# Kernel tuning notes

Hardware: AMD Instinct MI355X
Metric: run time of the kernel (lower is better)

## Reference

```python
import jax, jax.numpy as jnp
import numpy as np

N_NODES = 100000
N_EDGES = 1600000
IN_DIM, HID, OUT_DIM = 128, 64, 1


def _sage_conv(x, src, dst, wl, wr, b, num_nodes):
    # PyG SAGEConv (aggr='mean', root_weight=True):
    #   out = lin_l(mean_{j in N(i)} x_j) + lin_r(x_i), bias lives in lin_l
    msgs = x[src]                                                  # [E, d] gather
    agg = jax.ops.segment_sum(msgs, dst, num_segments=num_nodes)  # [N, d]
    deg = jax.ops.segment_sum(jnp.ones((src.shape[0],), x.dtype), dst,
                              num_segments=num_nodes)              # [N]
    agg = agg / jnp.maximum(deg, 1.0)[:, None]                     # mean aggregation
    return agg @ wl + x @ wr + b


def setup_inputs() -> dict:
    key = jax.random.key(0)
    ks = jax.random.split(key, 12)
    x = jax.random.normal(ks[0], (N_NODES, IN_DIM), dtype=jnp.float32)
    edge_index = jax.random.randint(ks[1], (2, N_EDGES), 0, N_NODES, dtype=jnp.int64)

    def glorot(k, fan_in, fan_out):
        s = jnp.sqrt(2.0 / (fan_in + fan_out)).astype(jnp.float32)
        return jax.random.normal(k, (fan_in, fan_out), dtype=jnp.float32) * s

    return {
        "x": x,
        "edge_index": edge_index,
        "wl0": glorot(ks[2], IN_DIM, HID), "wr0": glorot(ks[3], IN_DIM, HID),
        "b0": jnp.zeros((HID,), jnp.float32),
        "wl1": glorot(ks[4], HID, HID), "wr1": glorot(ks[5], HID, HID),
        "b1": jnp.zeros((HID,), jnp.float32),
        "wl2": glorot(ks[6], HID, OUT_DIM), "wr2": glorot(ks[7], HID, OUT_DIM),
        "b2": jnp.zeros((OUT_DIM,), jnp.float32),
    }


def reference(x, edge_index, wl0, wr0, b0, wl1, wr1, b1, wl2, wr2, b2):
    src, dst = edge_index[0], edge_index[1]
    n = x.shape[0]
    # layer 0: conv -> relu (dropout is identity in eval mode)
    h = jax.nn.relu(_sage_conv(x, src, dst, wl0, wr0, b0, n))
    # layer 1
    h = jax.nn.relu(_sage_conv(h, src, dst, wl1, wr1, b1, n))
    # final layer + sigmoid
    h = _sage_conv(h, src, dst, wl2, wr2, b2, n)
    return jax.nn.sigmoid(h)
```

## Files before the change

kernel.cpp:

```cpp
#include <hip/hip_runtime.h>
#include <hip/hip_bf16.h>
#include <math.h>


#define SHIFT 7
#define BKT 128
#define CHUNK 4096

typedef __bf16 bf16_t;
typedef bf16_t bf16x8 __attribute__((ext_vector_type(8)));
typedef float f32x4 __attribute__((ext_vector_type(4)));

#define B16LO(u) __uint_as_float((u) << 16)
#define B16HI(u) __uint_as_float((u) & 0xffff0000u)

__global__ __launch_bounds__(256) void hist_bucket(const int* __restrict__ dstv,
                                                   int* __restrict__ bucket_cnt,
                                                   int E, int NB, int nbC,
                                                   const float* __restrict__ wl0,
                                                   const float* __restrict__ wr0,
                                                   const float* __restrict__ wl1,
                                                   const float* __restrict__ wr1,
                                                   bf16_t* __restrict__ w0t,
                                                   bf16_t* __restrict__ w1t) {
    if ((int)blockIdx.x >= nbC) {
        int idx = (blockIdx.x - nbC) * 256 + threadIdx.x;
        if (idx < 128 * 128) {
            int j = idx >> 7, k = idx & 127;
            float v = (j < 64) ? wl0[k * 64 + j] : wr0[k * 64 + (j - 64)];
            w0t[idx] = (bf16_t)v;
        } else if (idx < 128 * 128 + 128 * 64) {
            int i2 = idx - 128 * 128;
            int j = i2 >> 6, k = i2 & 63;
            float v = (j < 64) ? wl1[k * 64 + j] : wr1[k * 64 + (j - 64)];
            w1t[i2] = (bf16_t)v;
        }
        return;
    }
    __shared__ int h[1024];
    for (int i = threadIdx.x; i < NB; i += 256) h[i] = 0;
    __syncthreads();
    int base = blockIdx.x * CHUNK;
#pragma unroll
    for (int k = 0; k < CHUNK / 256; ++k) {
        int e = base + threadIdx.x + k * 256;
        if (e < E) atomicAdd(&h[dstv[e] >> SHIFT], 1);
    }
    __syncthreads();
    for (int i = threadIdx.x; i < NB; i += 256)
        if (h[i]) atomicAdd(&bucket_cnt[i], h[i]);
}

__global__ __launch_bounds__(1024) void scan_bucket(const int* __restrict__ cnt,
                                                    int* __restrict__ boff,
                                                    int* __restrict__ bcur, int NB) {
    __shared__ int s[1024];
    int t = threadIdx.x;
    int v = (t < NB) ? cnt[t] : 0;
    s[t] = v;
    __syncthreads();
    for (int d = 1; d < 1024; d <<= 1) {
        int x = (t >= d) ? s[t - d] : 0;
        __syncthreads();
        s[t] += x;
        __syncthreads();
    }
    if (t < NB) {
        int o = s[t] - v;
        boff[t] = o;
        bcur[t] = o;
    }
    if (t == NB - 1) boff[NB] = s[t];
}

__global__ __launch_bounds__(256) void scatter_bucket(const int* __restrict__ srcv,
                                                      const int* __restrict__ dstv,
                                                      int* __restrict__ bcur,
                                                      int* __restrict__ bucketed,
                                                      int E, int NB) {
    __shared__ int hist[1024];
    __shared__ int offl[1024];
    __shared__ int basel[1024];
    __shared__ int partial[256];
    __shared__ int posA[CHUNK];
    __shared__ int valA[CHUNK];
    const int t = threadIdx.x;
    for (int i = t; i < NB; i += 256) hist[i] = 0;
    __syncthreads();

    const int cbase = blockIdx.x * CHUNK;
    int bk[CHUNK / 256], rk[CHUNK / 256], vv[CHUNK / 256];
#pragma unroll
    for (int k = 0; k < CHUNK / 256; ++k) {
        int e = cbase + t + k * 256;
        if (e < E) {
            int d = dstv[e];
            int s = srcv[e];
            int b = d >> SHIFT;
            bk[k] = b;
            rk[k] = atomicAdd(&hist[b], 1);
            vv[k] = (s << SHIFT) | (d & (BKT - 1));
        } else {
            bk[k] = -1;
        }
    }
    __syncthreads();

    for (int b = t; b < NB; b += 256) {
        int c = hist[b];
        basel[b] = c ? atomicAdd(&bcur[b], c) : 0;
    }
    {
        int g = t * 4;
        int a0 = (g + 0 < NB) ? hist[g + 0] : 0;
        int a1 = (g + 1 < NB) ? hist[g + 1] : 0;
        int a2 = (g + 2 < NB) ? hist[g + 2] : 0;
        int a3 = (g + 3 < NB) ? hist[g + 3] : 0;
        int sum = a0 + a1 + a2 + a3;
        partial[t] = sum;
        __syncthreads();
        for (int d = 1; d < 256; d <<= 1) {
            int x = (t >= d) ? partial[t - d] : 0;
            __syncthreads();
            partial[t] += x;
            __syncthreads();
        }
        int ex = partial[t] - sum;
        if (g + 0 < NB) offl[g + 0] = ex;
        if (g + 1 < NB) offl[g + 1] = ex + a0;
        if (g + 2 < NB) offl[g + 2] = ex + a0 + a1;
        if (g + 3 < NB) offl[g + 3] = ex + a0 + a1 + a2;
    }
    __syncthreads();

    int nloc = E - cbase;
    if (nloc > CHUNK) nloc = CHUNK;
#pragma unroll
    for (int k = 0; k < CHUNK / 256; ++k) {
        if (bk[k] >= 0) {
            int slot = offl[bk[k]] + rk[k];
            posA[slot] = basel[bk[k]] + rk[k];
            valA[slot] = vv[k];
        }
    }
    __syncthreads();
    for (int j = t; j < nloc; j += 256) bucketed[posA[j]] = valA[j];
}

__global__ __launch_bounds__(256) void sort_bucket(const int* __restrict__ bucketed,
                                                   const int* __restrict__ boff,
                                                   int2* __restrict__ od,
                                                   int* __restrict__ csr, int N) {
    __shared__ int cnt[BKT];
    __shared__ int sc[BKT];
    __shared__ int cur[BKT];
    const int b = blockIdx.x;
    const int t = threadIdx.x;
    const int ebase = boff[b], eend = boff[b + 1];
    if (t < BKT) cnt[t] = 0;
    __syncthreads();
    for (int i = ebase + t; i < eend; i += 256)
        atomicAdd(&cnt[bucketed[i] & (BKT - 1)], 1);
    __syncthreads();
    int v = (t < BKT) ? cnt[t] : 0;
    if (t < BKT) sc[t] = v;
    __syncthreads();
    for (int d = 1; d < BKT; d <<= 1) {
        int x = (t < BKT && t >= d) ? sc[t - d] : 0;
        __syncthreads();
        if (t < BKT) sc[t] += x;
        __syncthreads();
    }
    if (t < BKT) {
        int ex = sc[t] - v;
        cur[t] = ex;
        int dst = (b << SHIFT) + t;
        if (dst < N) od[dst] = make_int2(ebase + ex, v);
    }
    __syncthreads();
    for (int i = ebase + t; i < eend; i += 256) {
        int w = bucketed[i];
        int p = atomicAdd(&cur[w & (BKT - 1)], 1);
        csr[ebase + p] = w >> SHIFT;
    }
}

template <int KTOT, bool AIN_BF16>
__global__ __launch_bounds__(256) void gemm_mfma(const void* __restrict__ Ain,
                                                 const bf16_t* __restrict__ Wt,
                                                 bf16_t* __restrict__ Y, int N) {
    const int lane = threadIdx.x & 63;
    const int wv = threadIdx.x >> 6;
    const int r0 = blockIdx.x * 64 + wv * 16;
    const int rr = lane & 15;
    const int quad = lane >> 4;
    const int row_store = r0 + rr;
    int row = (row_store < N) ? row_store : (N - 1);
    constexpr int NK = KTOT / 32;

    bf16x8 xf[NK];
    if (AIN_BF16) {
        const bf16_t* A = (const bf16_t*)Ain;
#pragma unroll
        for (int kk = 0; kk < NK; ++kk)
            xf[kk] = *(const bf16x8*)&A[(size_t)row * KTOT + kk * 32 + quad * 8];
    } else {
        const float* A = (const float*)Ain;
#pragma unroll
        for (int kk = 0; kk < NK; ++kk) {
            const float* ap = &A[(size_t)row * KTOT + kk * 32 + quad * 8];
            float4 f0 = *(const float4*)ap;
            float4 f1 = *(const float4*)(ap + 4);
            union { bf16x8 v; bf16_t h[8]; } u;
            u.h[0] = (bf16_t)f0.x; u.h[1] = (bf16_t)f0.y;
            u.h[2] = (bf16_t)f0.z; u.h[3] = (bf16_t)f0.w;
            u.h[4] = (bf16_t)f1.x; u.h[5] = (bf16_t)f1.y;
            u.h[6] = (bf16_t)f1.z; u.h[7] = (bf16_t)f1.w;
            xf[kk] = u.v;
        }
    }

#pragma unroll
    for (int c = 0; c < 8; ++c) {
        f32x4 acc = {0.f, 0.f, 0.f, 0.f};
#pragma unroll
        for (int kk = 0; kk < NK; ++kk) {
            bf16x8 wf = *(const bf16x8*)&Wt[(size_t)(c * 16 + rr) * KTOT + kk * 32 + quad * 8];
            acc = __builtin_amdgcn_mfma_f32_16x16x32_bf16(wf, xf[kk], acc, 0, 0, 0);
        }
        if (row_store < N) {
            union { bf16_t h[4]; uint2 u; } p;
            p.h[0] = (bf16_t)acc[0]; p.h[1] = (bf16_t)acc[1];
            p.h[2] = (bf16_t)acc[2]; p.h[3] = (bf16_t)acc[3];
            *(uint2*)&Y[(size_t)row_store * 128 + c * 16 + quad * 4] = p.u;
        }
    }
}

template <bool FUSED>
__global__ __launch_bounds__(256) void agg_relu(const bf16_t* __restrict__ y,
                                                const int* __restrict__ csr,
                                                const int2* __restrict__ od,
                                                const float* __restrict__ bias,
                                                bf16_t* __restrict__ h,
                                                const float* __restrict__ wl2,
                                                const float* __restrict__ wr2,
                                                float* __restrict__ sl,
                                                float* __restrict__ sr, int N) {
    const int lane = threadIdx.x & 63;
    const int oct = lane >> 3;
    const int ch = (lane & 7) * 8;
    const int nw = gridDim.x * 4;

    int i = blockIdx.x * 4 + (threadIdx.x >> 6);
    int2 odc = (i < N) ? od[i] : make_int2(0, 0);
    int sidx = 0;
    if (i < N) sidx = (lane < odc.y) ? csr[odc.x + lane] : 0;

    while (i < N) {
        const int inext = i + nw;
        int2 odn = (inext < N) ? od[inext] : make_int2(0, 0);

        const int base = odc.x;
        const int d = odc.y;
        float a0 = 0.f, a1 = 0.f, a2 = 0.f, a3 = 0.f;
        float a4 = 0.f, a5 = 0.f, a6 = 0.f, a7 = 0.f;
        const int nblk = d >> 3;
        const int pm = (nblk < 8) ? nblk : 8;
        int p = 0;
        for (; p + 2 <= pm; p += 2) {
            int s0 = __shfl(sidx, 8 * p + oct);
            int s1 = __shfl(sidx, 8 * p + 8 + oct);
            uint4 v0 = *(const uint4*)&y[(size_t)s0 * 128 + ch];
            uint4 v1 = *(const uint4*)&y[(size_t)s1 * 128 + ch];
            a0 += B16LO(v0.x) + B16LO(v1.x); a1 += B16HI(v0.x) + B16HI(v1.x);
            a2 += B16LO(v0.y) + B16LO(v1.y); a3 += B16HI(v0.y) + B16HI(v1.y);
            a4 += B16LO(v0.z) + B16LO(v1.z); a5 += B16HI(v0.z) + B16HI(v1.z);
            a6 += B16LO(v0.w) + B16LO(v1.w); a7 += B16HI(v0.w) + B16HI(v1.w);
        }
        for (; p < pm; ++p) {
            int s0 = __shfl(sidx, 8 * p + oct);
            uint4 v0 = *(const uint4*)&y[(size_t)s0 * 128 + ch];
            a0 += B16LO(v0.x); a1 += B16HI(v0.x);
            a2 += B16LO(v0.y); a3 += B16HI(v0.y);
            a4 += B16LO(v0.z); a5 += B16HI(v0.z);
            a6 += B16LO(v0.w); a7 += B16HI(v0.w);
        }
        for (; p < nblk; ++p) {
            int s0 = csr[base + 8 * p + oct];
            uint4 v0 = *(const uint4*)&y[(size_t)s0 * 128 + ch];
            a0 += B16LO(v0.x); a1 += B16HI(v0.x);
            a2 += B16LO(v0.y); a3 += B16HI(v0.y);
            a4 += B16LO(v0.z); a5 += B16HI(v0.z);
            a6 += B16LO(v0.w); a7 += B16HI(v0.w);
        }
        {
            int te = 8 * nblk + oct;
            int tec = (te < 64) ? te : 63;
            int s_t = __shfl(sidx, tec);
            if (te < d) {
                int s0 = (te < 64) ? s_t : csr[base + te];
                uint4 v0 = *(const uint4*)&y[(size_t)s0 * 128 + ch];
                a0 += B16LO(v0.x); a1 += B16HI(v0.x);
                a2 += B16LO(v0.y); a3 += B16HI(v0.y);
                a4 += B16LO(v0.z); a5 += B16HI(v0.z);
                a6 += B16LO(v0.w); a7 += B16HI(v0.w);
            }
        }

        int sidxn = 0;
        if (inext < N) sidxn = (lane < odn.y) ? csr[odn.x + lane] : 0;

        a0 += __shfl_xor(a0, 8);  a1 += __shfl_xor(a1, 8);
        a2 += __shfl_xor(a2, 8);  a3 += __shfl_xor(a3, 8);
        a4 += __shfl_xor(a4, 8);  a5 += __shfl_xor(a5, 8);
        a6 += __shfl_xor(a6, 8);  a7 += __shfl_xor(a7, 8);
        a0 += __shfl_xor(a0, 16); a1 += __shfl_xor(a1, 16);
        a2 += __shfl_xor(a2, 16); a3 += __shfl_xor(a3, 16);
        a4 += __shfl_xor(a4, 16); a5 += __shfl_xor(a5, 16);
        a6 += __shfl_xor(a6, 16); a7 += __shfl_xor(a7, 16);
        a0 += __shfl_xor(a0, 32); a1 += __shfl_xor(a1, 32);
        a2 += __shfl_xor(a2, 32); a3 += __shfl_xor(a3, 32);
        a4 += __shfl_xor(a4, 32); a5 += __shfl_xor(a5, 32);
        a6 += __shfl_xor(a6, 32); a7 += __shfl_xor(a7, 32);

        float inv = 1.f / ((d > 0) ? (float)d : 1.f);
        uint4 vs = *(const uint4*)&y[(size_t)i * 128 + 64 + ch];
        float4 bv0 = *(const float4*)&bias[ch];
        float4 bv1 = *(const float4*)&bias[ch + 4];
        float v0 = fmaxf(a0 * inv + B16LO(vs.x) + bv0.x, 0.f);
        float v1 = fmaxf(a1 * inv + B16HI(vs.x) + bv0.y, 0.f);
        float v2 = fmaxf(a2 * inv + B16LO(vs.y) + bv0.z, 0.f);
        float v3 = fmaxf(a3 * inv + B16HI(vs.y) + bv0.w, 0.f);
        float v4 = fmaxf(a4 * inv + B16LO(vs.z) + bv1.x, 0.f);
        float v5 = fmaxf(a5 * inv + B16HI(vs.z) + bv1.y, 0.f);
        float v6 = fmaxf(a6 * inv + B16LO(vs.w) + bv1.z, 0.f);
        float v7 = fmaxf(a7 * inv + B16HI(vs.w) + bv1.w, 0.f);

        if (!FUSED) {
            if (oct == 0) {
                union { bf16_t b[8]; uint4 u; } pk;
                pk.b[0] = (bf16_t)v0; pk.b[1] = (bf16_t)v1;
                pk.b[2] = (bf16_t)v2; pk.b[3] = (bf16_t)v3;
                pk.b[4] = (bf16_t)v4; pk.b[5] = (bf16_t)v5;
                pk.b[6] = (bf16_t)v6; pk.b[7] = (bf16_t)v7;
                *(uint4*)&h[(size_t)i * 64 + ch] = pk.u;
            }
        } else {
            float4 w0 = *(const float4*)&wl2[ch];
            float4 w1 = *(const float4*)&wl2[ch + 4];
            float4 u0 = *(const float4*)&wr2[ch];
            float4 u1 = *(const float4*)&wr2[ch + 4];
            float a = v0 * w0.x + v1 * w0.y + v2 * w0.z + v3 * w0.w +
                      v4 * w1.x + v5 * w1.y + v6 * w1.z + v7 * w1.w;
            float b = v0 * u0.x + v1 * u0.y + v2 * u0.z + v3 * u0.w +
                      v4 * u1.x + v5 * u1.y + v6 * u1.z + v7 * u1.w;
            a += __shfl_xor(a, 1); b += __shfl_xor(b, 1);
            a += __shfl_xor(a, 2); b += __shfl_xor(b, 2);
            a += __shfl_xor(a, 4); b += __shfl_xor(b, 4);
            if (lane == 0) { sl[i] = a; sr[i] = b; }
        }

        odc = odn;
        sidx = sidxn;
        i = inext;
    }
}

__global__ __launch_bounds__(256) void final_k(const float* __restrict__ sl,
                                               const float* __restrict__ sr,
                                               const int* __restrict__ csr,
                                               const int2* __restrict__ od,
                                               const float* __restrict__ b2,
                                               float* __restrict__ out, int N) {
    int wid = blockIdx.x * 4 + (threadIdx.x >> 6);
    if (wid >= N) return;
    const int lane = threadIdx.x & 63;
    const int2 odv = od[wid];
    const int base = odv.x;
    const int d = odv.y;
    float acc = 0.f;
    for (int e = lane; e < d; e += 64) acc += sl[csr[base + e]];
#pragma unroll
    for (int off = 32; off; off >>= 1) acc += __shfl_xor(acc, off);
    if (lane == 0) {
        float m = (d > 0) ? (float)d : 1.f;
        float v = acc / m + sr[wid] + b2[0];
        out[wid] = 1.f / (1.f + expf(-v));
    }
}

extern "C" void kernel_launch(void* const* d_in, const int* in_sizes, int n_in,
                              void* d_out, int out_size, void* d_ws, size_t ws_size,
                              hipStream_t stream) {
    const float* x  = (const float*)d_in[0];
    const int*  ei  = (const int*)d_in[1];
    const float* wl0 = (const float*)d_in[2];
    const float* wr0 = (const float*)d_in[3];
    const float* b0  = (const float*)d_in[4];
    const float* wl1 = (const float*)d_in[5];
    const float* wr1 = (const float*)d_in[6];
    const float* b1  = (const float*)d_in[7];
    const float* wl2 = (const float*)d_in[8];
    const float* wr2 = (const float*)d_in[9];
    const float* b2  = (const float*)d_in[10];
    float* out = (float*)d_out;

    const int E = in_sizes[1] / 2;
    const int N = out_size;
    const int* srcv = ei;
    const int* dstv = ei + E;
    const int NB = (N + BKT - 1) >> SHIFT;

    char* ws = (char*)d_ws;
    size_t o = 0;
    auto take = [&](size_t nbytes) -> void* {
        void* p = ws + o;
        o = (o + nbytes + 255) & ~(size_t)255;
        return p;
    };
    int2* od    = (int2*)take((size_t)N * 8);
    int* bcnt   = (int*)take((size_t)(NB + 2) * 4);
    int* boff   = (int*)take((size_t)(NB + 2) * 4);
    int* bcur   = (int*)take((size_t)(NB + 2) * 4);
    int* csr    = (int*)take((size_t)E * 4);
    bf16_t* w0t = (bf16_t*)take(128 * 128 * 2);
    bf16_t* w1t = (bf16_t*)take(128 * 64 * 2);
    bf16_t* y   = (bf16_t*)take((size_t)N * 128 * 2);
    bf16_t* h   = (bf16_t*)take((size_t)N * 64 * 2);
    float* sl   = (float*)take((size_t)N * 4);
    float* sr   = (float*)take((size_t)N * 4);
    int* bucketed = (int*)y;
    (void)ws_size;

    const int nbC = (E + CHUNK - 1) / CHUNK;
    const int nbP = (128 * 128 + 128 * 64 + 255) / 256;
    const int nbW = (N + 3) / 4;
    const int nbG = (N + 63) / 64;
    const int nbA = 2048;

    hipMemsetAsync(bcnt, 0, (size_t)NB * 4, stream);
    hist_bucket<<<nbC + nbP, 256, 0, stream>>>(dstv, bcnt, E, NB, nbC,
                                               wl0, wr0, wl1, wr1, w0t, w1t);
    scan_bucket<<<1, 1024, 0, stream>>>(bcnt, boff, bcur, NB);
    scatter_bucket<<<nbC, 256, 0, stream>>>(srcv, dstv, bcur, bucketed, E, NB);
    sort_bucket<<<NB, 256, 0, stream>>>(bucketed, boff, od, csr, N);

    gemm_mfma<128, false><<<nbG, 256, 0, stream>>>((const void*)x, w0t, y, N);
    agg_relu<false><<<nbA, 256, 0, stream>>>(y, csr, od, b0, h,
                                             nullptr, nullptr, nullptr, nullptr, N);
    gemm_mfma<64, true><<<nbG, 256, 0, stream>>>((const void*)h, w1t, y, N);
    agg_relu<true><<<nbA, 256, 0, stream>>>(y, csr, od, b1, nullptr,
                                            wl2, wr2, sl, sr, N);
    final_k<<<nbW, 256, 0, stream>>>(sl, sr, csr, od, b2, out, N);
}
```

Before: 313.8 us.

## Split GEMM output into separate left/right arrays, add nontemporal loads, halve chunk

The GEMM output is split into two contiguous N×64 arrays, one for the neighbour (lin_l) half and one for the root (lin_r) half. The gather in agg_relu then reads a compact 128-byte row per neighbour instead of half of a 256-byte interleaved row, which should improve cache-line use and L2 footprint. Streaming index, offset and CSR accesses now use nontemporal loads and stores to reduce cache pollution. The bucketing CHUNK is halved, giving more blocks and less shared memory per block. Nontemporal hints on reused data such as csr and od could hurt reuse across kernels.

```diff
diff --git a/kernel.cpp b/kernel.cpp
--- a/kernel.cpp
+++ b/kernel.cpp
@@ -5,7 +5,7 @@
 
 #define SHIFT 7
 #define BKT 128
-#define CHUNK 4096
+#define CHUNK 2048
 
 typedef __bf16 bf16_t;
 typedef bf16_t bf16x8 __attribute__((ext_vector_type(8)));
@@ -13,6 +13,23 @@
 
 #define B16LO(u) __uint_as_float((u) << 16)
 #define B16HI(u) __uint_as_float((u) & 0xffff0000u)
+
+__device__ __forceinline__ int ntload_i(const int* p) {
+    return __builtin_nontemporal_load(p);
+}
+__device__ __forceinline__ int2 ntload_i2(const int2* p) {
+    long long v = __builtin_nontemporal_load((const long long*)p);
+    return make_int2((int)(v & 0xffffffffll), (int)(v >> 32));
+}
+__device__ __forceinline__ uint4 ntload_u4(const void* p) {
+    const unsigned long long* q = (const unsigned long long*)p;
+    unsigned long long a = __builtin_nontemporal_load(q);
+    unsigned long long b = __builtin_nontemporal_load(q + 1);
+    uint4 r;
+    r.x = (uint)a; r.y = (uint)(a >> 32);
+    r.z = (uint)b; r.w = (uint)(b >> 32);
+    return r;
+}
 
 __global__ __launch_bounds__(256) void hist_bucket(const int* __restrict__ dstv,
                                                    int* __restrict__ bucket_cnt,
@@ -44,7 +61,7 @@
 #pragma unroll
     for (int k = 0; k < CHUNK / 256; ++k) {
         int e = base + threadIdx.x + k * 256;
-        if (e < E) atomicAdd(&h[dstv[e] >> SHIFT], 1);
+        if (e < E) atomicAdd(&h[ntload_i(&dstv[e]) >> SHIFT], 1);
     }
     __syncthreads();
     for (int i = threadIdx.x; i < NB; i += 256)
@@ -94,8 +111,8 @@
     for (int k = 0; k < CHUNK / 256; ++k) {
         int e = cbase + t + k * 256;
         if (e < E) {
-            int d = dstv[e];
-            int s = srcv[e];
+            int d = ntload_i(&dstv[e]);
+            int s = ntload_i(&srcv[e]);
             int b = d >> SHIFT;
             bk[k] = b;
             rk[k] = atomicAdd(&hist[b], 1);
@@ -144,7 +161,8 @@
         }
     }
     __syncthreads();
-    for (int j = t; j < nloc; j += 256) bucketed[posA[j]] = valA[j];
+    for (int j = t; j < nloc; j += 256)
+        __builtin_nontemporal_store(valA[j], &bucketed[posA[j]]);
 }
 
 __global__ __launch_bounds__(256) void sort_bucket(const int* __restrict__ bucketed,
@@ -160,7 +178,7 @@
     if (t < BKT) cnt[t] = 0;
     __syncthreads();
     for (int i = ebase + t; i < eend; i += 256)
-        atomicAdd(&cnt[bucketed[i] & (BKT - 1)], 1);
+        atomicAdd(&cnt[ntload_i(&bucketed[i]) & (BKT - 1)], 1);
     __syncthreads();
     int v = (t < BKT) ? cnt[t] : 0;
     if (t < BKT) sc[t] = v;
@@ -179,16 +197,17 @@
     }
     __syncthreads();
     for (int i = ebase + t; i < eend; i += 256) {
-        int w = bucketed[i];
+        int w = ntload_i(&bucketed[i]);
         int p = atomicAdd(&cur[w & (BKT - 1)], 1);
-        csr[ebase + p] = w >> SHIFT;
+        __builtin_nontemporal_store(w >> SHIFT, &csr[ebase + p]);
     }
 }
 
 template <int KTOT, bool AIN_BF16>
 __global__ __launch_bounds__(256) void gemm_mfma(const void* __restrict__ Ain,
                                                  const bf16_t* __restrict__ Wt,
-                                                 bf16_t* __restrict__ Y, int N) {
+                                                 bf16_t* __restrict__ Yl,
+                                                 bf16_t* __restrict__ Yr, int N) {
     const int lane = threadIdx.x & 63;
     const int wv = threadIdx.x >> 6;
     const int r0 = blockIdx.x * 64 + wv * 16;
@@ -232,13 +251,17 @@
             union { bf16_t h[4]; uint2 u; } p;
             p.h[0] = (bf16_t)acc[0]; p.h[1] = (bf16_t)acc[1];
             p.h[2] = (bf16_t)acc[2]; p.h[3] = (bf16_t)acc[3];
-            *(uint2*)&Y[(size_t)row_store * 128 + c * 16 + quad * 4] = p.u;
+            int col = c * 16 + quad * 4;
+            bf16_t* dp = (c < 4) ? &Yl[(size_t)row_store * 64 + col]
+                                 : &Yr[(size_t)row_store * 64 + (col - 64)];
+            *(uint2*)dp = p.u;
         }
     }
 }
 
 template <bool FUSED>
-__global__ __launch_bounds__(256) void agg_relu(const bf16_t* __restrict__ y,
+__global__ __launch_bounds__(256) void agg_relu(const bf16_t* __restrict__ yl,
+                                                const bf16_t* __restrict__ yr,
                                                 const int* __restrict__ csr,
                                                 const int2* __restrict__ od,
                                                 const float* __restrict__ bias,
@@ -253,13 +276,13 @@
     const int nw = gridDim.x * 4;
 
     int i = blockIdx.x * 4 + (threadIdx.x >> 6);
-    int2 odc = (i < N) ? od[i] : make_int2(0, 0);
+    int2 odc = (i < N) ? ntload_i2(&od[i]) : make_int2(0, 0);
     int sidx = 0;
-    if (i < N) sidx = (lane < odc.y) ? csr[odc.x + lane] : 0;
+    if (i < N) sidx = (lane < odc.y) ? ntload_i(&csr[odc.x + lane]) : 0;
 
     while (i < N) {
         const int inext = i + nw;
-        int2 odn = (inext < N) ? od[inext] : make_int2(0, 0);
+        int2 odn = (inext < N) ? ntload_i2(&od[inext]) : make_int2(0, 0);
 
         const int base = odc.x;
         const int d = odc.y;
@@ -271,8 +294,8 @@
         for (; p + 2 <= pm; p += 2) {
             int s0 = __shfl(sidx, 8 * p + oct);
             int s1 = __shfl(sidx, 8 * p + 8 + oct);
-            uint4 v0 = *(const uint4*)&y[(size_t)s0 * 128 + ch];
-            uint4 v1 = *(const uint4*)&y[(size_t)s1 * 128 + ch];
+            uint4 v0 = *(const uint4*)&yl[(size_t)s0 * 64 + ch];
+            uint4 v1 = *(const uint4*)&yl[(size_t)s1 * 64 + ch];
             a0 += B16LO(v0.x) + B16LO(v1.x); a1 += B16HI(v0.x) + B16HI(v1.x);
             a2 += B16LO(v0.y) + B16LO(v1.y); a3 += B16HI(v0.y) + B16HI(v1.y);
             a4 += B16LO(v0.z) + B16LO(v1.z); a5 += B16HI(v0.z) + B16HI(v1.z);
@@ -280,15 +303,15 @@
         }
         for (; p < pm; ++p) {
             int s0 = __shfl(sidx, 8 * p + oct);
-            uint4 v0 = *(const uint4*)&y[(size_t)s0 * 128 + ch];
+            uint4 v0 = *(const uint4*)&yl[(size_t)s0 * 64 + ch];
             a0 += B16LO(v0.x); a1 += B16HI(v0.x);
             a2 += B16LO(v0.y); a3 += B16HI(v0.y);
             a4 += B16LO(v0.z); a5 += B16HI(v0.z);
             a6 += B16LO(v0.w); a7 += B16HI(v0.w);
         }
         for (; p < nblk; ++p) {
-            int s0 = csr[base + 8 * p + oct];
-            uint4 v0 = *(const uint4*)&y[(size_t)s0 * 128 + ch];
+            int s0 = ntload_i(&csr[base + 8 * p + oct]);
+            uint4 v0 = *(const uint4*)&yl[(size_t)s0 * 64 + ch];
             a0 += B16LO(v0.x); a1 += B16HI(v0.x);
             a2 += B16LO(v0.y); a3 += B16HI(v0.y);
             a4 += B16LO(v0.z); a5 += B16HI(v0.z);
@@ -299,8 +322,8 @@
             int tec = (te < 64) ? te : 63;
             int s_t = __shfl(sidx, tec);
             if (te < d) {
-                int s0 = (te < 64) ? s_t : csr[base + te];
-                uint4 v0 = *(const uint4*)&y[(size_t)s0 * 128 + ch];
+                int s0 = (te < 64) ? s_t : ntload_i(&csr[base + te]);
+                uint4 v0 = *(const uint4*)&yl[(size_t)s0 * 64 + ch];
                 a0 += B16LO(v0.x); a1 += B16HI(v0.x);
                 a2 += B16LO(v0.y); a3 += B16HI(v0.y);
                 a4 += B16LO(v0.z); a5 += B16HI(v0.z);
@@ -309,7 +332,7 @@
         }
 
         int sidxn = 0;
-        if (inext < N) sidxn = (lane < odn.y) ? csr[odn.x + lane] : 0;
+        if (inext < N) sidxn = (lane < odn.y) ? ntload_i(&csr[odn.x + lane]) : 0;
 
         a0 += __shfl_xor(a0, 8);  a1 += __shfl_xor(a1, 8);
         a2 += __shfl_xor(a2, 8);  a3 += __shfl_xor(a3, 8);
@@ -325,7 +348,7 @@
         a6 += __shfl_xor(a6, 32); a7 += __shfl_xor(a7, 32);
 
         float inv = 1.f / ((d > 0) ? (float)d : 1.f);
-        uint4 vs = *(const uint4*)&y[(size_t)i * 128 + 64 + ch];
+        uint4 vs = ntload_u4(&yr[(size_t)i * 64 + ch]);
         float4 bv0 = *(const float4*)&bias[ch];
         float4 bv1 = *(const float4*)&bias[ch + 4];
         float v0 = fmaxf(a0 * inv + B16LO(vs.x) + bv0.x, 0.f);
@@ -344,7 +367,9 @@
                 pk.b[2] = (bf16_t)v2; pk.b[3] = (bf16_t)v3;
                 pk.b[4] = (bf16_t)v4; pk.b[5] = (bf16_t)v5;
                 pk.b[6] = (bf16_t)v6; pk.b[7] = (bf16_t)v7;
-                *(uint4*)&h[(size_t)i * 64 + ch] = pk.u;
+                unsigned long long* hp = (unsigned long long*)&h[(size_t)i * 64 + ch];
+                __builtin_nontemporal_store(((unsigned long long)pk.u.y << 32) | pk.u.x, hp);
+                __builtin_nontemporal_store(((unsigned long long)pk.u.w << 32) | pk.u.z, hp + 1);
             }
         } else {
             float4 w0 = *(const float4*)&wl2[ch];
@@ -376,11 +401,11 @@
     int wid = blockIdx.x * 4 + (threadIdx.x >> 6);
     if (wid >= N) return;
     const int lane = threadIdx.x & 63;
-    const int2 odv = od[wid];
+    const int2 odv = ntload_i2(&od[wid]);
     const int base = odv.x;
     const int d = odv.y;
     float acc = 0.f;
-    for (int e = lane; e < d; e += 64) acc += sl[csr[base + e]];
+    for (int e = lane; e < d; e += 64) acc += sl[ntload_i(&csr[base + e])];
 #pragma unroll
     for (int off = 32; off; off >>= 1) acc += __shfl_xor(acc, off);
     if (lane == 0) {
@@ -426,11 +451,12 @@
     int* csr    = (int*)take((size_t)E * 4);
     bf16_t* w0t = (bf16_t*)take(128 * 128 * 2);
     bf16_t* w1t = (bf16_t*)take(128 * 64 * 2);
-    bf16_t* y   = (bf16_t*)take((size_t)N * 128 * 2);
+    bf16_t* yl  = (bf16_t*)take((size_t)N * 64 * 2);
+    bf16_t* yr  = (bf16_t*)take((size_t)N * 64 * 2);
     bf16_t* h   = (bf16_t*)take((size_t)N * 64 * 2);
     float* sl   = (float*)take((size_t)N * 4);
     float* sr   = (float*)take((size_t)N * 4);
-    int* bucketed = (int*)y;
+    int* bucketed = (int*)yl;
     (void)ws_size;
 
     const int nbC = (E + CHUNK - 1) / CHUNK;
@@ -446,11 +472,11 @@
     scatter_bucket<<<nbC, 256, 0, stream>>>(srcv, dstv, bcur, bucketed, E, NB);
     sort_bucket<<<NB, 256, 0, stream>>>(bucketed, boff, od, csr, N);
 
-    gemm_mfma<128, false><<<nbG, 256, 0, stream>>>((const void*)x, w0t, y, N);
-    agg_relu<false><<<nbA, 256, 0, stream>>>(y, csr, od, b0, h,
+    gemm_mfma<128, false><<<nbG, 256, 0, stream>>>((const void*)x, w0t, yl, yr, N);
+    agg_relu<false><<<nbA, 256, 0, stream>>>(yl, yr, csr, od, b0, h,
                                              nullptr, nullptr, nullptr, nullptr, N);
-    gemm_mfma<64, true><<<nbG, 256, 0, stream>>>((const void*)h, w1t, y, N);
-    agg_relu<true><<<nbA, 256, 0, stream>>>(y, csr, od, b1, nullptr,
+    gemm_mfma<64, true><<<nbG, 256, 0, stream>>>((const void*)h, w1t, yl, yr, N);
+    agg_relu<true><<<nbA, 256, 0, stream>>>(yl, yr, csr, od, b1, nullptr,
                                             wl2, wr2, sl, sr, N);
     final_k<<<nbW, 256, 0, stream>>>(sl, sr, csr, od, b2, out, N);
 }
```

Result: slower. 378.5 us (+20.6%).
